# Performance work log

Hardware: AMD Instinct MI355X
Metric: run time of the kernel (lower is better)

Reference implementation:

```python
import jax, jax.numpy as jnp
import numpy as np
import math

D_MODEL = 1024; NHEAD = 16; HEAD_DIM = D_MODEL // NHEAD
MOE_HIDDEN = 2048; NUM_EXPERTS = 4; TOP_K = 2
DECOMP_KS = (7, 25, 49)
B = 8; N = 1024
LN_EPS = 1e-5

def _alibi_slopes(n):
    start = 2.0 ** (-2.0 ** (-(math.log2(n) - 3)))
    return np.array([start * (start ** i) for i in range(n)], dtype=np.float32)

ALIBI = jnp.asarray(_alibi_slopes(NHEAD))  # [H]

def setup_inputs() -> dict:
    key = jax.random.key(0)
    ks = jax.random.split(key, 16)
    rn = lambda k, s, sc=0.02: jax.random.normal(k, s, dtype=jnp.float32) * sc
    z = lambda s: jnp.zeros(s, jnp.float32)
    inp = {}
    inp['x'] = jax.random.normal(ks[0], (B, N, D_MODEL), dtype=jnp.float32)
    inp['qw'] = rn(ks[1], (D_MODEL, D_MODEL)); inp['qb'] = z((D_MODEL,))
    inp['kw'] = rn(ks[2], (D_MODEL, D_MODEL)); inp['kb'] = z((D_MODEL,))
    inp['vw'] = rn(ks[3], (D_MODEL, D_MODEL)); inp['vb'] = z((D_MODEL,))
    inp['ow'] = rn(ks[4], (D_MODEL, D_MODEL)); inp['ob'] = z((D_MODEL,))
    inp['n1g'] = jnp.ones((D_MODEL,), jnp.float32); inp['n1b'] = z((D_MODEL,))
    inp['n2g'] = jnp.ones((D_MODEL,), jnp.float32); inp['n2b'] = z((D_MODEL,))
    inp['alpha'] = z((len(DECOMP_KS),))
    # depthwise moving-average kernels (module inits to 1/k); add jitter so grads are non-trivial
    inp['dw7'] = jnp.full((D_MODEL, 1, 7), 1.0 / 7, jnp.float32) + rn(ks[5], (D_MODEL, 1, 7), 0.01)
    inp['dw25'] = jnp.full((D_MODEL, 1, 25), 1.0 / 25, jnp.float32) + rn(ks[6], (D_MODEL, 1, 25), 0.01)
    inp['dw49'] = jnp.full((D_MODEL, 1, 49), 1.0 / 49, jnp.float32) + rn(ks[7], (D_MODEL, 1, 49), 0.01)
    inp['router_w'] = rn(ks[8], (NUM_EXPERTS, D_MODEL))
    inp['ew1'] = rn(ks[9], (NUM_EXPERTS, MOE_HIDDEN, D_MODEL)); inp['eb1'] = z((NUM_EXPERTS, MOE_HIDDEN))
    inp['ew2'] = rn(ks[10], (NUM_EXPERTS, D_MODEL, MOE_HIDDEN)); inp['eb2'] = z((NUM_EXPERTS, D_MODEL))
    inp['tw'] = rn(ks[11], (D_MODEL, 1, 5)); inp['tb'] = z((D_MODEL,))
    return inp

def _ln(x, g, b):
    m = jnp.mean(x, axis=-1, keepdims=True)
    v = jnp.mean((x - m) ** 2, axis=-1, keepdims=True)
    return (x - m) * jax.lax.rsqrt(v + LN_EPS) * g + b

def _dwconv(x_bdn, w):  # depthwise 1D conv, VALID padding; w: [D,1,k]
    return jax.lax.conv_general_dilated(
        x_bdn, w, window_strides=(1,), padding='VALID',
        feature_group_count=D_MODEL, dimension_numbers=('NCH', 'OIH', 'NCH'))

def _forward(x, qw, qb, kw, kb, vw, vb, ow, ob, n1g, n1b, n2g, n2b,
             alpha, dw7, dw25, dw49, router_w, ew1, eb1, ew2, eb2, tw, tb):
    # ---- Decomp1D: multi-kernel depthwise moving averages, softmax-mixed ----
    xt = jnp.transpose(x, (0, 2, 1))  # [B, D, N]
    trends = []
    for w_, k in zip((dw7, dw25, dw49), DECOMP_KS):
        xp = jnp.pad(xt, ((0, 0), (0, 0), (k // 2, k // 2)), mode='reflect')
        trends.append(_dwconv(xp, w_))  # [B, D, N]
    wts = jax.nn.softmax(alpha)
    Tr = sum(wi * ti for wi, ti in zip(wts, trends))  # trend [B, D, N]
    Tr = jnp.transpose(Tr, (0, 2, 1))  # [B, N, D]
    S = x - Tr                          # seasonal
    # ---- ALiBi self-attention on normalized seasonal part ----
    Sn = _ln(S, n1g, n1b)
    split = lambda h: jnp.transpose(h.reshape(B, N, NHEAD, HEAD_DIM), (0, 2, 1, 3))
    q = split(Sn @ qw.T + qb)
    k = split(Sn @ kw.T + kb)
    v = split(Sn @ vw.T + vb)
    logits = jnp.einsum('bhqd,bhkd->bhqk', q, k) / math.sqrt(HEAD_DIM)
    idx = jnp.arange(N)
    dist = jnp.clip(idx[None, :] - idx[:, None], 0, None).astype(jnp.float32)  # (j-i)+
    logits = logits - ALIBI[None, :, None, None] * dist[None, None]
    attn = jax.nn.softmax(logits, axis=-1)
    y = jnp.einsum('bhqk,bhkd->bhqd', attn, v)
    y = jnp.transpose(y, (0, 2, 1, 3)).reshape(B, N, D_MODEL) @ ow.T + ob
    x_s = S + y
    # ---- top-2 gated MoE FFN (no capacity limit) ----
    xf = _ln(x_s, n2g, n2b).reshape(B * N, D_MODEL)
    gates = jax.nn.softmax(xf @ router_w.T, axis=-1)  # [T, E]
    topv, topi = jax.lax.top_k(gates, TOP_K)
    topv = topv / jnp.clip(jnp.sum(topv, axis=-1, keepdims=True), 1e-9, None)
    weights = jnp.zeros_like(gates).at[jnp.arange(B * N)[:, None], topi].set(topv)
    aux = NUM_EXPERTS * jnp.sum(jnp.mean(gates, axis=0) *
                                jnp.mean((weights > 0).astype(jnp.float32), axis=0))
    out = jnp.zeros_like(xf)
    for e in range(NUM_EXPERTS):  # small fixed expert count
        h = jax.nn.gelu(xf @ ew1[e].T + eb1[e], approximate=False)
        out = out + (h @ ew2[e].T + eb2[e]) * weights[:, e:e + 1]
    x_s = x_s + out.reshape(B, N, D_MODEL)
    # ---- trend depthwise conv (k=5, zero padding=2, bias) ----
    tp = jnp.pad(jnp.transpose(Tr, (0, 2, 1)), ((0, 0), (0, 0), (2, 2)))
    t_out = _dwconv(tp, tw) + tb[None, :, None]
    return (x_s + jnp.transpose(t_out, (0, 2, 1)), aux)

def reference(x, qw, qb, kw, kb, vw, vb, ow, ob, n1g, n1b, n2g, n2b,
              alpha, dw7, dw25, dw49, router_w, ew1, eb1, ew2, eb2, tw, tb):
    return _forward(x, qw, qb, kw, kb, vw, vb, ow, ob, n1g, n1b, n2g, n2b,
                    alpha, dw7, dw25, dw49, router_w, ew1, eb1, ew2, eb2, tw, tb)
```

## Files before the change

### kernel.cpp

```cpp
#include <hip/hip_runtime.h>
#include <hip/hip_bf16.h>
#include <math.h>

using bf16 = __hip_bfloat16;
typedef __attribute__((ext_vector_type(8))) short s8v;
typedef __attribute__((ext_vector_type(4))) float f32x4;

#define D_MODEL 1024
#define NB 8
#define SEQ 1024
#define NHEAD 16
#define HD 64
#define MOE_H 2048
#define TOKENS (NB*SEQ)
#define QKV_S 3072

__global__ void f2b_k(const float* __restrict__ in, bf16* __restrict__ out, int n) {
    int i = blockIdx.x * blockDim.x + threadIdx.x;
    int stride = gridDim.x * blockDim.x;
    for (; i < n; i += stride) out[i] = __float2bfloat16(in[i]);
}

__global__ void cat3_k(const float* __restrict__ a, const float* __restrict__ b,
                       const float* __restrict__ c, float* __restrict__ o) {
    int i = blockIdx.x * blockDim.x + threadIdx.x;
    if (i < 1024) o[i] = a[i];
    else if (i < 2048) o[i] = b[i - 1024];
    else if (i < 3072) o[i] = c[i - 2048];
}

__global__ void prefix_k(const int* __restrict__ cnt, int* __restrict__ off) {
    if (threadIdx.x == 0 && blockIdx.x == 0) {
        int s = 0;
        for (int e = 0; e < 4; e++) { off[e] = s; s += cnt[e]; }
    }
}

#define TN 128
#define TD 64
__global__ __launch_bounds__(256) void decomp_k(
    const float* __restrict__ x, const float* __restrict__ alpha,
    const float* __restrict__ dw7, const float* __restrict__ dw25,
    const float* __restrict__ dw49, float* __restrict__ Tr, float* __restrict__ S)
{
    __shared__ float xs[TN + 48][TD];
    const int n0 = blockIdx.x * TN, d0 = blockIdx.y * TD, b = blockIdx.z;
    for (int i = threadIdx.x; i < (TN + 48) * (TD / 4); i += 256) {
        int r = i / (TD / 4), c4 = (i % (TD / 4)) * 4;
        int n = n0 + r - 24;
        if (n < 0) n = -n;
        if (n > SEQ - 1) n = 2 * (SEQ - 1) - n;
        *(float4*)&xs[r][c4] =
            *(const float4*)&x[((size_t)(b * SEQ + n)) * D_MODEL + d0 + c4];
    }
    float a0 = alpha[0], a1 = alpha[1], a2 = alpha[2];
    float mx = fmaxf(a0, fmaxf(a1, a2));
    float e0 = __expf(a0 - mx), e1 = __expf(a1 - mx), e2 = __expf(a2 - mx);
    float inv = 1.0f / (e0 + e1 + e2);
    float w7 = e0 * inv, w25 = e1 * inv, w49 = e2 * inv;
    const int dl = threadIdx.x & 63;
    const int nt = threadIdx.x >> 6;
    const int d = d0 + dl;
    float w[49];
    #pragma unroll
    for (int j = 0; j < 49; j++) {
        float v = w49 * dw49[d * 49 + j];
        if (j >= 12 && j < 37) v += w25 * dw25[d * 25 + j - 12];
        if (j >= 21 && j < 28) v += w7 * dw7[d * 7 + j - 21];
        w[j] = v;
    }
    __syncthreads();
    for (int nl = nt; nl < TN; nl += 4) {
        float acc = 0.f;
        #pragma unroll
        for (int j = 0; j < 49; j++) acc = fmaf(xs[nl + j][dl], w[j], acc);
        size_t idx = ((size_t)(b * SEQ + n0 + nl)) * D_MODEL + d;
        Tr[idx] = acc;
        S[idx] = xs[nl + 24][dl] - acc;
    }
}

__global__ __launch_bounds__(256) void ln_k(
    const float* __restrict__ x, const float* __restrict__ g, const float* __restrict__ b,
    bf16* __restrict__ ob, float* __restrict__ of)
{
    int row = blockIdx.x, t = threadIdx.x;
    const float* xr = x + (size_t)row * D_MODEL;
    float s = 0.f, s2 = 0.f;
    for (int d = t; d < D_MODEL; d += 256) { float v = xr[d]; s += v; s2 += v * v; }
    #pragma unroll
    for (int o = 32; o > 0; o >>= 1) { s += __shfl_down(s, o); s2 += __shfl_down(s2, o); }
    __shared__ float sh[8];
    int wid = t >> 6, lane = t & 63;
    if (lane == 0) { sh[wid] = s; sh[4 + wid] = s2; }
    __syncthreads();
    if (t == 0) {
        float ts = sh[0] + sh[1] + sh[2] + sh[3];
        float t2 = sh[4] + sh[5] + sh[6] + sh[7];
        float m = ts / D_MODEL;
        float var = t2 / D_MODEL - m * m;
        sh[0] = m; sh[1] = rsqrtf(var + 1e-5f);
    }
    __syncthreads();
    float m = sh[0], rs = sh[1];
    for (int d = t; d < D_MODEL; d += 256) {
        float v = (xr[d] - m) * rs * g[d] + b[d];
        ob[(size_t)row * D_MODEL + d] = __float2bfloat16(v);
        if (of) of[(size_t)row * D_MODEL + d] = v;
    }
}

template<int ACT, int OMODE, int GMODE>
__global__ __launch_bounds__(512, 4) void gemm_nt(
    const bf16* __restrict__ A, const bf16* __restrict__ B,
    const float* __restrict__ bias, const float* resid,
    const float* __restrict__ rowscale, int rs_stride,
    void* C, int M, int K, int O,
    const int* __restrict__ row_map, const int* __restrict__ cnt_ptr,
    const int* __restrict__ off_ptr, size_t b_estride, int bias_estride)
{
    const int bm = blockIdx.x, bn = blockIdx.y;
    const int e = (GMODE != 0) ? blockIdx.z : 0;
    int M_act = M;
    int off = 0;
    const int* rmap = row_map;
    if (GMODE != 0) {
        M_act = cnt_ptr[e];
        if (bm * 128 >= M_act) return;
        off = off_ptr[e];
        rmap = row_map + e * TOKENS;
        B += (size_t)e * b_estride;
        if (bias) bias += (size_t)e * bias_estride;
    }
    __shared__ bf16 As[2][128][72];
    __shared__ bf16 Bs[2][128][72];
    const int t = threadIdx.x;
    const int lane = t & 63, wid = t >> 6;
    const int wm = wid >> 1, wn = wid & 1;
    f32x4 acc[2][4] = {};
    const int lr = t >> 3;
    const int lc = (t & 7) * 8;
    const size_t abase = (GMODE == 2) ? (size_t)(off + bm * 128) * K : (size_t)(bm * 128) * K;
    const size_t bbase = (size_t)(bn * 128) * K;
    size_t arow[2];
    #pragma unroll
    for (int p = 0; p < 2; p++) {
        int r = p * 64 + lr;
        if (GMODE == 1) {
            int gr = bm * 128 + r;
            arow[p] = (size_t)rmap[gr < M_act ? gr : M_act - 1] * K;
        } else {
            arow[p] = abase + (size_t)r * K;
        }
    }
    const int nt = K / 64;

#define LOADT(RA, RB, TT) do { const int kn_ = (TT) * 64 + lc;                      \
    _Pragma("unroll") for (int p_ = 0; p_ < 2; p_++) {                              \
        RA[p_] = *(const s8v*)&A[arow[p_] + kn_];                                   \
        RB[p_] = *(const s8v*)&B[bbase + (size_t)(p_ * 64 + lr) * K + kn_]; } } while (0)
#define WRITET(BUF, RA, RB) do {                                                    \
    _Pragma("unroll") for (int p_ = 0; p_ < 2; p_++) {                              \
        *(s8v*)&As[BUF][p_ * 64 + lr][lc] = RA[p_];                                 \
        *(s8v*)&Bs[BUF][p_ * 64 + lr][lc] = RB[p_]; } } while (0)
#define LBAR() do { asm volatile("s_waitcnt lgkmcnt(0)" ::: "memory");              \
    __builtin_amdgcn_sched_barrier(0); __builtin_amdgcn_s_barrier(); } while (0)
#define COMPUTE(BUF) do {                                                           \
    _Pragma("unroll") for (int kk_ = 0; kk_ < 64; kk_ += 32) {                      \
        s8v af_[2], bf_[4];                                                         \
        _Pragma("unroll") for (int i_ = 0; i_ < 2; i_++)                            \
            af_[i_] = *(const s8v*)&As[BUF][wm * 32 + i_ * 16 + fr][kk_ + fq];      \
        _Pragma("unroll") for (int j_ = 0; j_ < 4; j_++)                            \
            bf_[j_] = *(const s8v*)&Bs[BUF][wn * 64 + j_ * 16 + fr][kk_ + fq];      \
        _Pragma("unroll") for (int i_ = 0; i_ < 2; i_++)                            \
            _Pragma("unroll") for (int j_ = 0; j_ < 4; j_++)                        \
                acc[i_][j_] = __builtin_amdgcn_mfma_f32_16x16x32_bf16(af_[i_], bf_[j_], acc[i_][j_], 0, 0, 0); \
    } } while (0)

    const int fr = lane & 15, fq = (lane >> 4) * 8;
    s8v r0a[2], r0b[2], r1a[2], r1b[2];
    LOADT(r0a, r0b, 0);
    WRITET(0, r0a, r0b);
    LOADT(r1a, r1b, 1);
    LOADT(r0a, r0b, 2);
    LBAR();

    for (int tt = 0; tt < nt; tt += 2) {
        WRITET(1, r1a, r1b);
        if (tt + 3 < nt) LOADT(r1a, r1b, tt + 3);
        COMPUTE(0);
        LBAR();
        if (tt + 2 < nt) {
            WRITET(0, r0a, r0b);
            if (tt + 4 < nt) LOADT(r0a, r0b, tt + 4);
        }
        COMPUTE(1);
        LBAR();
    }
#undef LOADT
#undef WRITET
#undef LBAR
#undef COMPUTE

    const int cr = lane & 15, quad = lane >> 4;
    #pragma unroll
    for (int i = 0; i < 2; i++) {
        #pragma unroll
        for (int r = 0; r < 4; r++) {
            int row = bm * 128 + wm * 32 + i * 16 + quad * 4 + r;
            if (GMODE != 0 && row >= M_act) continue;
            int srow = (GMODE == 2) ? rmap[row] : ((GMODE == 1) ? off + row : row);
            #pragma unroll
            for (int j = 0; j < 4; j++) {
                int col = bn * 128 + wn * 64 + j * 16 + cr;
                float v = acc[i][j][r];
                if (bias) v += bias[col];
                if (ACT == 1) v = 0.5f * v * (1.0f + erff(v * 0.70710678118f));
                size_t idx = (size_t)srow * O + col;
                if (OMODE == 0) {
                    float rv = resid ? resid[idx] : 0.0f;
                    ((float*)C)[idx] = rv + v;
                } else if (OMODE == 1) {
                    ((bf16*)C)[idx] = __float2bfloat16(v);
                } else {
                    atomicAdd(&((float*)C)[idx], rowscale[(size_t)srow * rs_stride + e] * v);
                }
            }
        }
    }
}

__global__ __launch_bounds__(256) void attn_k(
    const bf16* __restrict__ QKV, bf16* __restrict__ Y)
{
    __shared__ bf16 Ks[64][72];
    __shared__ bf16 Vt[64][66];
    __shared__ bf16 Pw[4][32][72];
    const int t = threadIdx.x;
    const int wave = t >> 6, lane = t & 63;
    const int qm = lane & 15, quad = lane >> 4;
    const int b = blockIdx.z, h = blockIdx.y;
    const int qbase = blockIdx.x * 128 + wave * 32;
    const float LOG2E = 1.44269504f;
    const float slope2 = exp2f(-0.5f * (float)(h + 1)) * LOG2E;
    const float NEG8L2 = -11.54156036f;
    const float SCL2   = 0.18033688f;

    s8v qa[2][2];
    #pragma unroll
    for (int g = 0; g < 2; g++) {
        const bf16* qp = QKV + ((size_t)(b * SEQ + qbase + g * 16 + qm)) * QKV_S + h * HD;
        qa[g][0] = *(const s8v*)&qp[quad * 8];
        qa[g][1] = *(const s8v*)&qp[32 + quad * 8];
    }
    float aqp[2][4];
    #pragma unroll
    for (int g = 0; g < 2; g++)
        #pragma unroll
        for (int r = 0; r < 4; r++)
            aqp[g][r] = slope2 * (float)(qbase + g * 16 + quad * 4 + r) + NEG8L2;

    f32x4 o[2][4] = {};
    float l[2][4] = {};

    const int sr = t >> 2;
    const int scc = (t & 3) * 16;
    const bf16* kvb = QKV + (size_t)(b * SEQ) * QKV_S + D_MODEL + h * HD + scc;

    {
        const bf16* p0 = kvb + (size_t)sr * QKV_S;
        s8v k0v = *(const s8v*)&p0[0];
        s8v k1v = *(const s8v*)&p0[8];
        s8v v0  = *(const s8v*)&p0[D_MODEL];
        s8v v1  = *(const s8v*)&p0[D_MODEL + 8];

        for (int k0 = 0; k0 < SEQ; k0 += 64) {
            *(s8v*)&Ks[sr][scc] = k0v;
            *(s8v*)&Ks[sr][scc + 8] = k1v;
            #pragma unroll
            for (int j = 0; j < 8; j++) {
                Vt[scc + j][sr]     = ((const bf16*)&v0)[j];
                Vt[scc + 8 + j][sr] = ((const bf16*)&v1)[j];
            }
            __syncthreads();
            if (k0 + 64 < SEQ) {
                const bf16* np = kvb + (size_t)(k0 + 64 + sr) * QKV_S;
                k0v = *(const s8v*)&np[0];
                k1v = *(const s8v*)&np[8];
                v0  = *(const s8v*)&np[D_MODEL];
                v1  = *(const s8v*)&np[D_MODEL + 8];
            }
            float bk[4];
            #pragma unroll
            for (int jt = 0; jt < 4; jt++) bk[jt] = slope2 * (float)(k0 + jt * 16 + qm);
            #pragma unroll
            for (int g = 0; g < 2; g++) {
                f32x4 scr[4];
                #pragma unroll
                for (int jt = 0; jt < 4; jt++) {
                    f32x4 z = {};
                    s8v b0 = *(const s8v*)&Ks[jt * 16 + qm][quad * 8];
                    s8v b1 = *(const s8v*)&Ks[jt * 16 + qm][32 + quad * 8];
                    z = __builtin_amdgcn_mfma_f32_16x16x32_bf16(qa[g][0], b0, z, 0, 0, 0);
                    z = __builtin_amdgcn_mfma_f32_16x16x32_bf16(qa[g][1], b1, z, 0, 0, 0);
                    scr[jt] = z;
                }
                #pragma unroll
                for (int jt = 0; jt < 4; jt++) {
                    #pragma unroll
                    for (int r = 0; r < 4; r++) {
                        float term = fminf(aqp[g][r] - bk[jt], NEG8L2);
                        float pf = exp2f(fmaf(scr[jt][r], SCL2, term));
                        bf16 pb = __float2bfloat16(pf);
                        l[g][r] += __bfloat162float(pb);
                        Pw[wave][g * 16 + quad * 4 + r][jt * 16 + qm] = pb;
                    }
                }
            }
            __builtin_amdgcn_wave_barrier();
            #pragma unroll
            for (int g = 0; g < 2; g++) {
                s8v pa0 = *(const s8v*)&Pw[wave][g * 16 + qm][quad * 8];
                s8v pa1 = *(const s8v*)&Pw[wave][g * 16 + qm][32 + quad * 8];
                #pragma unroll
                for (int dt = 0; dt < 4; dt++) {
                    s8v vb0 = *(const s8v*)&Vt[dt * 16 + qm][quad * 8];
                    s8v vb1 = *(const s8v*)&Vt[dt * 16 + qm][32 + quad * 8];
                    o[g][dt] = __builtin_amdgcn_mfma_f32_16x16x32_bf16(pa0, vb0, o[g][dt], 0, 0, 0);
                    o[g][dt] = __builtin_amdgcn_mfma_f32_16x16x32_bf16(pa1, vb1, o[g][dt], 0, 0, 0);
                }
            }
            __syncthreads();
        }
    }
    #pragma unroll
    for (int g = 0; g < 2; g++)
        #pragma unroll
        for (int r = 0; r < 4; r++) {
            float s = l[g][r];
            s += __shfl_xor(s, 1); s += __shfl_xor(s, 2);
            s += __shfl_xor(s, 4); s += __shfl_xor(s, 8);
            l[g][r] = 1.0f / s;
        }
    #pragma unroll
    for (int g = 0; g < 2; g++)
        #pragma unroll
        for (int dt = 0; dt < 4; dt++)
            #pragma unroll
            for (int r = 0; r < 4; r++) {
                size_t idx = ((size_t)(b * SEQ + qbase + g * 16 + quad * 4 + r)) * D_MODEL + h * HD + dt * 16 + qm;
                Y[idx] = __float2bfloat16(o[g][dt][r] * l[g][r]);
            }
}

__global__ __launch_bounds__(256) void router_k(
    const float* __restrict__ xf, const float* __restrict__ rw,
    float* __restrict__ wts, float* __restrict__ auxb,
    int* __restrict__ cnt, int* __restrict__ elist)
{
    const int wave = threadIdx.x >> 6, lane = threadIdx.x & 63;
    float4 w[4][4];
    #pragma unroll
    for (int e = 0; e < 4; e++)
        #pragma unroll
        for (int c = 0; c < 4; c++)
            w[e][c] = *(const float4*)&rw[e * D_MODEL + lane * 16 + c * 4];
    float ag[4] = {0.f, 0.f, 0.f, 0.f};
    float ac[4] = {0.f, 0.f, 0.f, 0.f};
    __shared__ int sel[16][2];
    __shared__ float sh[4][8];
    const int t0 = (blockIdx.x * 4 + wave) * 4;
    #pragma unroll
    for (int i = 0; i < 4; i++) {
        const int tk = t0 + i;
        const float* xr = xf + (size_t)tk * D_MODEL + lane * 16;
        float4 xv[4];
        #pragma unroll
        for (int c = 0; c < 4; c++) xv[c] = *(const float4*)&xr[c * 4];
        float p[4] = {0.f, 0.f, 0.f, 0.f};
        #pragma unroll
        for (int e = 0; e < 4; e++)
            #pragma unroll
            for (int c = 0; c < 4; c++) {
                p[e] = fmaf(xv[c].x, w[e][c].x, p[e]);
                p[e] = fmaf(xv[c].y, w[e][c].y, p[e]);
                p[e] = fmaf(xv[c].z, w[e][c].z, p[e]);
                p[e] = fmaf(xv[c].w, w[e][c].w, p[e]);
            }
        #pragma unroll
        for (int o = 1; o < 64; o <<= 1) {
            p[0] += __shfl_xor(p[0], o); p[1] += __shfl_xor(p[1], o);
            p[2] += __shfl_xor(p[2], o); p[3] += __shfl_xor(p[3], o);
        }
        float g[4];
        float mx = fmaxf(fmaxf(p[0], p[1]), fmaxf(p[2], p[3]));
        float se = 0.f;
        #pragma unroll
        for (int e = 0; e < 4; e++) { g[e] = __expf(p[e] - mx); se += g[e]; }
        #pragma unroll
        for (int e = 0; e < 4; e++) g[e] /= se;
        int i1 = 0; float v1 = g[0];
        #pragma unroll
        for (int e = 1; e < 4; e++) if (g[e] > v1) { v1 = g[e]; i1 = e; }
        int i2 = -1; float v2 = -1.f;
        #pragma unroll
        for (int e = 0; e < 4; e++) if (e != i1 && g[e] > v2) { v2 = g[e]; i2 = e; }
        float sw = fmaxf(v1 + v2, 1e-9f);
        if (lane < 4) {
            float wv = (lane == i1) ? v1 / sw : ((lane == i2) ? v2 / sw : 0.f);
            wts[(size_t)tk * 4 + lane] = wv;
        }
        if (lane == 0) {
            #pragma unroll
            for (int e = 0; e < 4; e++) ag[e] += g[e];
            ac[i1] += 1.f; ac[i2] += 1.f;
            sel[wave * 4 + i][0] = i1;
            sel[wave * 4 + i][1] = i2;
        }
    }
    if (lane == 0)
        #pragma unroll
        for (int e = 0; e < 4; e++) { sh[wave][e] = ag[e]; sh[wave][4 + e] = ac[e]; }
    __syncthreads();
    if (threadIdx.x < 8) {
        float s = sh[0][threadIdx.x] + sh[1][threadIdx.x] + sh[2][threadIdx.x] + sh[3][threadIdx.x];
        atomicAdd(&auxb[threadIdx.x], s);
    }
    if (threadIdx.x < 4) {
        const int e = threadIdx.x;
        int loc[16]; int c = 0;
        #pragma unroll
        for (int s = 0; s < 16; s++)
            if (sel[s][0] == e || sel[s][1] == e) loc[c++] = blockIdx.x * 16 + s;
        if (c) {
            int base = atomicAdd(&cnt[e], c);
            for (int k = 0; k < c; k++) elist[e * TOKENS + base + k] = loc[k];
        }
    }
}

__global__ __launch_bounds__(256) void final_k(
    const float* __restrict__ xs, const float* __restrict__ Tr,
    const float* __restrict__ tw, const float* __restrict__ tb, float* __restrict__ out)
{
    int n = blockIdx.x, b = blockIdx.y, t = threadIdx.x;
    for (int d = t; d < D_MODEL; d += 256) {
        float acc = tb[d];
        #pragma unroll
        for (int j = 0; j < 5; j++) {
            int i = n + j - 2;
            if (i >= 0 && i < SEQ)
                acc += Tr[((size_t)(b * SEQ + i)) * D_MODEL + d] * tw[d * 5 + j];
        }
        size_t idx = ((size_t)(b * SEQ + n)) * D_MODEL + d;
        out[idx] = xs[idx] + acc;
    }
}

__global__ void aux_k(const float* __restrict__ ab, float* __restrict__ out) {
    if (threadIdx.x == 0 && blockIdx.x == 0) {
        float a = 0.f;
        for (int e = 0; e < 4; e++)
            a += (ab[e] / (float)TOKENS) * (ab[4 + e] / (float)TOKENS);
        out[0] = 4.0f * a;
    }
}

extern "C" void kernel_launch(void* const* d_in, const int* in_sizes, int n_in,
                              void* d_out, int out_size, void* d_ws, size_t ws_size,
                              hipStream_t stream)
{
    const float* x    = (const float*)d_in[0];
    const float* qw   = (const float*)d_in[1];
    const float* qb   = (const float*)d_in[2];
    const float* kw   = (const float*)d_in[3];
    const float* kb   = (const float*)d_in[4];
    const float* vw   = (const float*)d_in[5];
    const float* vb   = (const float*)d_in[6];
    const float* ow   = (const float*)d_in[7];
    const float* ob   = (const float*)d_in[8];
    const float* n1g  = (const float*)d_in[9];
    const float* n1b  = (const float*)d_in[10];
    const float* n2g  = (const float*)d_in[11];
    const float* n2b  = (const float*)d_in[12];
    const float* alpha= (const float*)d_in[13];
    const float* dw7  = (const float*)d_in[14];
    const float* dw25 = (const float*)d_in[15];
    const float* dw49 = (const float*)d_in[16];
    const float* rw   = (const float*)d_in[17];
    const float* ew1  = (const float*)d_in[18];
    const float* eb1  = (const float*)d_in[19];
    const float* ew2  = (const float*)d_in[20];
    const float* eb2  = (const float*)d_in[21];
    const float* tw   = (const float*)d_in[22];
    const float* tb   = (const float*)d_in[23];

    char* ws = (char*)d_ws;
    const size_t MBy = 1ull << 20;
    float* S    = (float*)(ws + 0 * MBy);
    float* Tr   = (float*)(ws + 32 * MBy);
    float* XF   = (float*)(ws + 64 * MBy);
    bf16*  SNB  = (bf16*)(ws + 96 * MBy);
    bf16*  QKVB = (bf16*)(ws + 112 * MBy);
    bf16*  XFB  = (bf16*)(ws + 160 * MBy);
    bf16*  WQ   = (bf16*)(ws + 176 * MBy);
    bf16*  WK   = (bf16*)(ws + 178 * MBy);
    bf16*  WV   = (bf16*)(ws + 180 * MBy);
    bf16*  WO   = (bf16*)(ws + 182 * MBy);
    bf16*  WE1  = (bf16*)(ws + 184 * MBy);
    bf16*  WE2  = (bf16*)(ws + 200 * MBy);
    float* WTS  = (float*)(ws + 216 * MBy);
    float* AUXB = (float*)(ws + 217 * MBy);
    int*   CNT  = (int*)(AUXB + 8);
    int*   OFF  = CNT + 4;
    float* QKVBIAS = (float*)(ws + 217 * MBy + 4096);
    int*   ELST = (int*)(ws + 218 * MBy);
    bf16*  YB = SNB;
    bf16*  HALL = (bf16*)(ws + 96 * MBy);

    f2b_k<<<2048, 256, 0, stream>>>(qw, WQ, D_MODEL * D_MODEL);
    f2b_k<<<2048, 256, 0, stream>>>(kw, WK, D_MODEL * D_MODEL);
    f2b_k<<<2048, 256, 0, stream>>>(vw, WV, D_MODEL * D_MODEL);
    f2b_k<<<2048, 256, 0, stream>>>(ow, WO, D_MODEL * D_MODEL);
    f2b_k<<<4096, 256, 0, stream>>>(ew1, WE1, 4 * MOE_H * D_MODEL);
    f2b_k<<<4096, 256, 0, stream>>>(ew2, WE2, 4 * D_MODEL * MOE_H);
    cat3_k<<<12, 256, 0, stream>>>(qb, kb, vb, QKVBIAS);

    decomp_k<<<dim3(SEQ / TN, D_MODEL / TD, NB), 256, 0, stream>>>(x, alpha, dw7, dw25, dw49, Tr, S);

    ln_k<<<TOKENS, 256, 0, stream>>>(S, n1g, n1b, SNB, nullptr);

    gemm_nt<0, 1, 0><<<dim3(64, 24), 512, 0, stream>>>(SNB, WQ, QKVBIAS, nullptr, nullptr, 0, QKVB, TOKENS, D_MODEL, QKV_S, nullptr, nullptr, nullptr, 0, 0);

    attn_k<<<dim3(SEQ / 128, NHEAD, NB), 256, 0, stream>>>(QKVB, YB);

    gemm_nt<0, 0, 0><<<dim3(64, 8), 512, 0, stream>>>(YB, WO, ob, S, nullptr, 0, S, TOKENS, D_MODEL, D_MODEL, nullptr, nullptr, nullptr, 0, 0);

    ln_k<<<TOKENS, 256, 0, stream>>>(S, n2g, n2b, XFB, XF);

    hipMemsetAsync(AUXB, 0, 64, stream);
    router_k<<<TOKENS / 16, 256, 0, stream>>>(XF, rw, WTS, AUXB, CNT, ELST);
    prefix_k<<<1, 64, 0, stream>>>(CNT, OFF);

    gemm_nt<1, 1, 1><<<dim3(64, MOE_H / 128, 4), 512, 0, stream>>>(
        XFB, WE1, eb1, nullptr, nullptr, 0, HALL, TOKENS, D_MODEL, MOE_H,
        ELST, CNT, OFF, (size_t)MOE_H * D_MODEL, MOE_H);
    gemm_nt<0, 2, 2><<<dim3(64, D_MODEL / 128, 4), 512, 0, stream>>>(
        HALL, WE2, eb2, nullptr, WTS, 4, S, TOKENS, MOE_H, D_MODEL,
        ELST, CNT, OFF, (size_t)D_MODEL * MOE_H, D_MODEL);

    final_k<<<dim3(SEQ, NB), 256, 0, stream>>>(S, Tr, tw, tb, (float*)d_out);
    aux_k<<<1, 64, 0, stream>>>(AUXB, (float*)d_out + (out_size - 1));
}
```

Before: 858.5 us.

## Replace MoE down-proj atomic scatter with bf16 output plus per-token combine; merge weight casts

The second expert GEMM no longer scatters through atomicAdd into the residual. It writes a contiguous bf16 output per expert slot, and a new combine kernel gathers each token's two expert rows using a reverse index built by the router, applies the gate weights and adds them to S. The change is meant to remove atomic contention and the scattered fp32 read-modify-writes, at the cost of an extra kernel and a 16 MB bf16 intermediate round trip. The six weight-cast launches are also merged into one kernel to reduce launch overhead. The expert output is now rounded to bf16 before the weighted sum, which slightly changes numerics.

```diff
diff --git a/kernel.cpp b/kernel.cpp
--- a/kernel.cpp
+++ b/kernel.cpp
@@ -15,10 +15,24 @@
 #define TOKENS (NB*SEQ)
 #define QKV_S 3072
 
-__global__ void f2b_k(const float* __restrict__ in, bf16* __restrict__ out, int n) {
-    int i = blockIdx.x * blockDim.x + threadIdx.x;
-    int stride = gridDim.x * blockDim.x;
-    for (; i < n; i += stride) out[i] = __float2bfloat16(in[i]);
+__global__ void f2b_all(const float* __restrict__ s0, const float* __restrict__ s1,
+                        const float* __restrict__ s2, const float* __restrict__ s3,
+                        const float* __restrict__ s4, const float* __restrict__ s5,
+                        bf16* __restrict__ d0, bf16* __restrict__ d1,
+                        bf16* __restrict__ d2, bf16* __restrict__ d3,
+                        bf16* __restrict__ d4, bf16* __restrict__ d5)
+{
+    const size_t M1 = 1024 * 1024;
+    const size_t total = 4 * M1 + 8 * M1 + 8 * M1;
+    for (size_t i = (size_t)blockIdx.x * blockDim.x + threadIdx.x; i < total;
+         i += (size_t)gridDim.x * blockDim.x) {
+        if (i < M1)            d0[i] = __float2bfloat16(s0[i]);
+        else if (i < 2 * M1)   d1[i - M1] = __float2bfloat16(s1[i - M1]);
+        else if (i < 3 * M1)   d2[i - 2 * M1] = __float2bfloat16(s2[i - 2 * M1]);
+        else if (i < 4 * M1)   d3[i - 3 * M1] = __float2bfloat16(s3[i - 3 * M1]);
+        else if (i < 12 * M1)  d4[i - 4 * M1] = __float2bfloat16(s4[i - 4 * M1]);
+        else                   d5[i - 12 * M1] = __float2bfloat16(s5[i - 12 * M1]);
+    }
 }
 
 __global__ void cat3_k(const float* __restrict__ a, const float* __restrict__ b,
@@ -114,7 +128,6 @@
 __global__ __launch_bounds__(512, 4) void gemm_nt(
     const bf16* __restrict__ A, const bf16* __restrict__ B,
     const float* __restrict__ bias, const float* resid,
-    const float* __restrict__ rowscale, int rs_stride,
     void* C, int M, int K, int O,
     const int* __restrict__ row_map, const int* __restrict__ cnt_ptr,
     const int* __restrict__ off_ptr, size_t b_estride, int bias_estride)
@@ -128,7 +141,7 @@
         M_act = cnt_ptr[e];
         if (bm * 128 >= M_act) return;
         off = off_ptr[e];
-        rmap = row_map + e * TOKENS;
+        if (GMODE == 1) rmap = row_map + e * TOKENS;
         B += (size_t)e * b_estride;
         if (bias) bias += (size_t)e * bias_estride;
     }
@@ -209,7 +222,7 @@
         for (int r = 0; r < 4; r++) {
             int row = bm * 128 + wm * 32 + i * 16 + quad * 4 + r;
             if (GMODE != 0 && row >= M_act) continue;
-            int srow = (GMODE == 2) ? rmap[row] : ((GMODE == 1) ? off + row : row);
+            int srow = (GMODE != 0) ? off + row : row;
             #pragma unroll
             for (int j = 0; j < 4; j++) {
                 int col = bn * 128 + wn * 64 + j * 16 + cr;
@@ -220,14 +233,35 @@
                 if (OMODE == 0) {
                     float rv = resid ? resid[idx] : 0.0f;
                     ((float*)C)[idx] = rv + v;
-                } else if (OMODE == 1) {
+                } else {
                     ((bf16*)C)[idx] = __float2bfloat16(v);
-                } else {
-                    atomicAdd(&((float*)C)[idx], rowscale[(size_t)srow * rs_stride + e] * v);
                 }
             }
         }
     }
+}
+
+__global__ __launch_bounds__(256) void combine_k(
+    const bf16* __restrict__ H, const int* __restrict__ rev,
+    const int* __restrict__ offp, const float* __restrict__ wts,
+    float* __restrict__ S)
+{
+    const int tk = blockIdx.x, t = threadIdx.x;
+    const int r0 = rev[tk * 2], r1 = rev[tk * 2 + 1];
+    const int e0 = r0 >> 13, e1 = r1 >> 13;
+    const float w0 = wts[tk * 4 + e0], w1 = wts[tk * 4 + e1];
+    const bf16* h0 = H + (size_t)(offp[e0] + (r0 & 8191)) * D_MODEL;
+    const bf16* h1 = H + (size_t)(offp[e1] + (r1 & 8191)) * D_MODEL;
+    float* sr = S + (size_t)tk * D_MODEL;
+    const int d = t * 4;
+    ushort4 a = *(const ushort4*)&h0[d];
+    ushort4 b = *(const ushort4*)&h1[d];
+    float4 sv = *(float4*)&sr[d];
+    sv.x += w0 * __bfloat162float(*(const bf16*)&a.x) + w1 * __bfloat162float(*(const bf16*)&b.x);
+    sv.y += w0 * __bfloat162float(*(const bf16*)&a.y) + w1 * __bfloat162float(*(const bf16*)&b.y);
+    sv.z += w0 * __bfloat162float(*(const bf16*)&a.z) + w1 * __bfloat162float(*(const bf16*)&b.z);
+    sv.w += w0 * __bfloat162float(*(const bf16*)&a.w) + w1 * __bfloat162float(*(const bf16*)&b.w);
+    *(float4*)&sr[d] = sv;
 }
 
 __global__ __launch_bounds__(256) void attn_k(
@@ -356,7 +390,7 @@
 __global__ __launch_bounds__(256) void router_k(
     const float* __restrict__ xf, const float* __restrict__ rw,
     float* __restrict__ wts, float* __restrict__ auxb,
-    int* __restrict__ cnt, int* __restrict__ elist)
+    int* __restrict__ cnt, int* __restrict__ elist, int* __restrict__ rev)
 {
     const int wave = threadIdx.x >> 6, lane = threadIdx.x & 63;
     float4 w[4][4];
@@ -431,10 +465,16 @@
         int loc[16]; int c = 0;
         #pragma unroll
         for (int s = 0; s < 16; s++)
-            if (sel[s][0] == e || sel[s][1] == e) loc[c++] = blockIdx.x * 16 + s;
+            if (sel[s][0] == e || sel[s][1] == e) loc[c++] = s;
         if (c) {
             int base = atomicAdd(&cnt[e], c);
-            for (int k = 0; k < c; k++) elist[e * TOKENS + base + k] = loc[k];
+            for (int k = 0; k < c; k++) {
+                int s = loc[k];
+                int tok = blockIdx.x * 16 + s;
+                elist[e * TOKENS + base + k] = tok;
+                int slot = (sel[s][0] == e) ? 0 : 1;
+                rev[tok * 2 + slot] = (e << 13) | (base + k);
+            }
         }
     }
 }
@@ -500,6 +540,7 @@
     float* S    = (float*)(ws + 0 * MBy);
     float* Tr   = (float*)(ws + 32 * MBy);
     float* XF   = (float*)(ws + 64 * MBy);
+    bf16*  HOUT = (bf16*)(ws + 64 * MBy);
     bf16*  SNB  = (bf16*)(ws + 96 * MBy);
     bf16*  QKVB = (bf16*)(ws + 112 * MBy);
     bf16*  XFB  = (bf16*)(ws + 160 * MBy);
@@ -515,39 +556,36 @@
     int*   OFF  = CNT + 4;
     float* QKVBIAS = (float*)(ws + 217 * MBy + 4096);
     int*   ELST = (int*)(ws + 218 * MBy);
+    int*   REV  = (int*)(ws + 218 * MBy + 131072);
     bf16*  YB = SNB;
     bf16*  HALL = (bf16*)(ws + 96 * MBy);
 
-    f2b_k<<<2048, 256, 0, stream>>>(qw, WQ, D_MODEL * D_MODEL);
-    f2b_k<<<2048, 256, 0, stream>>>(kw, WK, D_MODEL * D_MODEL);
-    f2b_k<<<2048, 256, 0, stream>>>(vw, WV, D_MODEL * D_MODEL);
-    f2b_k<<<2048, 256, 0, stream>>>(ow, WO, D_MODEL * D_MODEL);
-    f2b_k<<<4096, 256, 0, stream>>>(ew1, WE1, 4 * MOE_H * D_MODEL);
-    f2b_k<<<4096, 256, 0, stream>>>(ew2, WE2, 4 * D_MODEL * MOE_H);
+    f2b_all<<<4096, 256, 0, stream>>>(qw, kw, vw, ow, ew1, ew2, WQ, WK, WV, WO, WE1, WE2);
     cat3_k<<<12, 256, 0, stream>>>(qb, kb, vb, QKVBIAS);
 
     decomp_k<<<dim3(SEQ / TN, D_MODEL / TD, NB), 256, 0, stream>>>(x, alpha, dw7, dw25, dw49, Tr, S);
 
     ln_k<<<TOKENS, 256, 0, stream>>>(S, n1g, n1b, SNB, nullptr);
 
-    gemm_nt<0, 1, 0><<<dim3(64, 24), 512, 0, stream>>>(SNB, WQ, QKVBIAS, nullptr, nullptr, 0, QKVB, TOKENS, D_MODEL, QKV_S, nullptr, nullptr, nullptr, 0, 0);
+    gemm_nt<0, 1, 0><<<dim3(64, 24), 512, 0, stream>>>(SNB, WQ, QKVBIAS, nullptr, QKVB, TOKENS, D_MODEL, QKV_S, nullptr, nullptr, nullptr, 0, 0);
 
     attn_k<<<dim3(SEQ / 128, NHEAD, NB), 256, 0, stream>>>(QKVB, YB);
 
-    gemm_nt<0, 0, 0><<<dim3(64, 8), 512, 0, stream>>>(YB, WO, ob, S, nullptr, 0, S, TOKENS, D_MODEL, D_MODEL, nullptr, nullptr, nullptr, 0, 0);
+    gemm_nt<0, 0, 0><<<dim3(64, 8), 512, 0, stream>>>(YB, WO, ob, S, S, TOKENS, D_MODEL, D_MODEL, nullptr, nullptr, nullptr, 0, 0);
 
     ln_k<<<TOKENS, 256, 0, stream>>>(S, n2g, n2b, XFB, XF);
 
     hipMemsetAsync(AUXB, 0, 64, stream);
-    router_k<<<TOKENS / 16, 256, 0, stream>>>(XF, rw, WTS, AUXB, CNT, ELST);
+    router_k<<<TOKENS / 16, 256, 0, stream>>>(XF, rw, WTS, AUXB, CNT, ELST, REV);
     prefix_k<<<1, 64, 0, stream>>>(CNT, OFF);
 
     gemm_nt<1, 1, 1><<<dim3(64, MOE_H / 128, 4), 512, 0, stream>>>(
-        XFB, WE1, eb1, nullptr, nullptr, 0, HALL, TOKENS, D_MODEL, MOE_H,
+        XFB, WE1, eb1, nullptr, HALL, TOKENS, D_MODEL, MOE_H,
         ELST, CNT, OFF, (size_t)MOE_H * D_MODEL, MOE_H);
-    gemm_nt<0, 2, 2><<<dim3(64, D_MODEL / 128, 4), 512, 0, stream>>>(
-        HALL, WE2, eb2, nullptr, WTS, 4, S, TOKENS, MOE_H, D_MODEL,
-        ELST, CNT, OFF, (size_t)D_MODEL * MOE_H, D_MODEL);
+    gemm_nt<0, 1, 2><<<dim3(64, D_MODEL / 128, 4), 512, 0, stream>>>(
+        HALL, WE2, eb2, nullptr, HOUT, TOKENS, MOE_H, D_MODEL,
+        nullptr, CNT, OFF, (size_t)D_MODEL * MOE_H, D_MODEL);
+    combine_k<<<TOKENS, 256, 0, stream>>>(HOUT, REV, OFF, WTS, S);
 
     final_k<<<dim3(SEQ, NB), 256, 0, stream>>>(S, Tr, tw, tb, (float*)d_out);
     aux_k<<<1, 64, 0, stream>>>(AUXB, (float*)d_out + (out_size - 1));
```

Result: no change. 856.4 us (-0.3%).
